# Optimization experiments

Measured on AMD Instinct MI355X. Metric: run time of the kernel, lower is better.

The kernel has to match this reference:

```python
import jax, jax.numpy as jnp
import numpy as np

B, T, F = 16, 2048, 512


def setup_inputs() -> dict:
    key = jax.random.key(0)
    k1, k2, k3 = jax.random.split(key, 3)
    x = jax.random.normal(k1, (B, T, F), dtype=jnp.float32)
    w_aggr = jax.random.normal(k2, (F, 1), dtype=jnp.float32) * 0.02
    b_aggr = jnp.zeros((1,), dtype=jnp.float32)
    # lengths in [T//2, T] to avoid degenerate lengths[0]==0 (torch would div by 0 too)
    seq_len = jax.random.randint(k3, (B,), T // 2, T + 1).astype(jnp.int32)
    return {"x": x, "w_aggr": w_aggr, "b_aggr": b_aggr, "seq_len": seq_len}


def reference(x, w_aggr, b_aggr, seq_len):
    """Valley-detection dynamic segment-mean pooling.

    Faithful to the torch code, but the O(T^2) triangular-mask bmm is
    expressed as the mathematically identical prefix-sum difference:
    bmm(utri[end]-utri[start], v) == cumsum(v)[end] - cumsum(v)[start].
    Output time dim is padded to T (>= dynamic max_counts); padded segment
    rows have start==end==0 -> numerator 0 / clamp -> exactly 0, matching
    the torch zero-padded `valleys` rows.
    """
    Bx, Tx, Fx = x.shape
    wt = jax.nn.sigmoid(x @ w_aggr + b_aggr)[..., 0]          # [B,T] gate weights
    before = jnp.pad(wt[:, :-1], ((0, 0), (1, 0)))            # pad 0 (sigmoid>0 => pos 0 never valley)
    after = jnp.pad(wt[:, 1:], ((0, 0), (0, 1)))              # pad 0 => pos T-1 never valley
    valley = (wt < before) & (wt < after)                     # [B,T] strict local minima
    starts_mask = valley.at[:, 0].set(True)                   # mask[:,0]=True
    ends_mask = valley.at[:, 0].set(False).at[:, -1].set(True)  # mask[:,0]=False; mask[:,-1]=True

    t = jnp.arange(Tx, dtype=jnp.int32)
    bi = jnp.arange(Bx)[:, None]

    def pack(m, vals):
        # left-pack values at True positions into fixed [B,T] (zeros beyond count)
        rank = jnp.cumsum(m, axis=1) - 1
        slot = jnp.where(m, rank, Tx)                         # dump non-selected into slot T
        out = jnp.zeros((Bx, Tx + 1), jnp.int32).at[bi, slot].set(vals)
        return out[:, :Tx], jnp.sum(m, axis=1)

    starts, counts = pack(starts_mask, jnp.broadcast_to(t, (Bx, Tx)))
    end_vals = jnp.broadcast_to(jnp.minimum(t + 2, Tx), (Bx, Tx))  # valley_index_end clipped to length
    ends, _ = pack(ends_mask, end_vals)

    alpha_h = wt[..., None] * x                               # [B,T,F]
    # exclusive->inclusive prefix sums with leading zero row
    cs_ah = jnp.concatenate([jnp.zeros((Bx, 1, Fx), x.dtype), jnp.cumsum(alpha_h, axis=1)], axis=1)
    cs_w = jnp.concatenate([jnp.zeros((Bx, 1), x.dtype), jnp.cumsum(wt, axis=1)], axis=1)

    num = cs_ah[bi, ends] - cs_ah[bi, starts]                 # [B,T,F] segment sums of w*x
    den = jnp.clip(cs_w[bi, ends] - cs_w[bi, starts], 1e-6, None)[..., None]
    pooled = num / den                                        # weighted segment mean

    max_counts = jnp.max(counts)
    lengths = jnp.minimum(seq_len, Tx)
    new_lengths = (lengths.astype(jnp.float32) / lengths[0].astype(jnp.float32)
                   * max_counts.astype(jnp.float32)).astype(jnp.int32)
    new_mask = t[None, :] < new_lengths[:, None]              # [B,T]
    return pooled, new_mask
```

## Files before the change

kernel.cpp:

```cpp
#include <hip/hip_runtime.h>
#include <math.h>

#define BB 16
#define TT 2048
#define FF 512

#define ACTIVE_BLOCKS 4096
#define ZERO_BLOCKS   1024
#define MASK_BLOCKS   32

typedef float v4f __attribute__((ext_vector_type(4)));

__global__ __launch_bounds__(256) void wt_kernel(const float* __restrict__ x,
                                                 const float* __restrict__ w,
                                                 const float* __restrict__ bias,
                                                 float* __restrict__ wt) {
    int gid  = blockIdx.x * 256 + threadIdx.x;
    int row  = gid >> 6;
    int lane = gid & 63;
    const float* xr = x + (size_t)row * FF + lane * 8;
    const float* wr = w + lane * 8;
    float4 a0 = *(const float4*)xr;
    float4 a1 = *(const float4*)(xr + 4);
    float4 w0 = *(const float4*)wr;
    float4 w1 = *(const float4*)(wr + 4);
    float s = a0.x * w0.x + a0.y * w0.y + a0.z * w0.z + a0.w * w0.w
            + a1.x * w1.x + a1.y * w1.y + a1.z * w1.z + a1.w * w1.w;
#pragma unroll
    for (int off = 32; off > 0; off >>= 1) s += __shfl_xor(s, off, 64);
    if (lane == 0) {
        float z = s + bias[0];
        wt[row] = 1.0f / (1.0f + expf(-z));
    }
}

__global__ __launch_bounds__(64) void seg_kernel(const float* __restrict__ wt,
                                                 int* __restrict__ starts,
                                                 int* __restrict__ ends,
                                                 int* __restrict__ counts) {
    int b    = blockIdx.x;
    int lane = threadIdx.x;
    const float* wrow = wt + b * TT;
    float v[32];
    const float4* p = (const float4*)(wrow + lane * 32);
#pragma unroll
    for (int k = 0; k < 8; ++k) {
        float4 f = p[k];
        v[4*k] = f.x; v[4*k+1] = f.y; v[4*k+2] = f.z; v[4*k+3] = f.w;
    }
    float left  = __shfl_up(v[31], 1, 64);
    float right = __shfl_down(v[0], 1, 64);
    unsigned int flags = 0;
#pragma unroll
    for (int k = 0; k < 32; ++k) {
        int t = lane * 32 + k;
        float prev = (k == 0)  ? left  : v[k - 1];
        float next = (k == 31) ? right : v[k + 1];
        bool val = (t > 0) && (t < TT - 1) && (v[k] < prev) && (v[k] < next);
        if (val) flags |= (1u << k);
    }
    int cnt = __popc(flags);
    int inc = cnt;
#pragma unroll
    for (int off = 1; off < 64; off <<= 1) {
        int y = __shfl_up(inc, off, 64);
        if (lane >= off) inc += y;
    }
    int total = __shfl(inc, 63, 64);
    int r = inc - cnt;
    int* sb = starts + b * TT;
    int* eb = ends + b * TT;
    unsigned int f = flags;
    while (f) {
        int k = __ffs(f) - 1;
        f &= f - 1;
        int t = lane * 32 + k;
        sb[r + 1] = t;
        eb[r] = t + 2;
        ++r;
    }
    if (lane == 0) {
        sb[0] = 0;
        eb[total] = TT;
        counts[b] = total + 1;
    }
}

__global__ __launch_bounds__(256) void pool_kernel(const float* __restrict__ x,
                                                   const float* __restrict__ wt,
                                                   const int* __restrict__ starts,
                                                   const int* __restrict__ ends,
                                                   const int* __restrict__ counts,
                                                   const int* __restrict__ seq_len,
                                                   float* __restrict__ out,
                                                   float* __restrict__ mask_out) {
    int blk = blockIdx.x;
    int tid = threadIdx.x;
    v4f zero = (v4f)(0.f);

    if (blk >= ACTIVE_BLOCKS + ZERO_BLOCKS) {
        int idx = (blk - ACTIVE_BLOCKS - ZERO_BLOCKS) * 256 + tid;
        int maxc = 0;
#pragma unroll
        for (int i = 0; i < BB; ++i) maxc = max(maxc, counts[i]);
        float len0 = (float)min(seq_len[0], TT);
#pragma unroll
        for (int r = 0; r < 4; ++r) {
            int i = idx + r * 8192;
            int b = i >> 11, t = i & (TT - 1);
            int nl = (int)((float)min(seq_len[b], TT) / len0 * (float)maxc);
            mask_out[i] = (t < nl) ? 1.0f : 0.0f;
        }
        return;
    }

    if (blk >= ACTIVE_BLOCKS) {
        int zb = blk - ACTIVE_BLOCKS;
        int b  = zb >> 6;
        int j0 = 1024 + (zb & 63) * 16;
        float* base = out + ((size_t)(b * TT + j0) * FF);
        v4f* dst = (v4f*)base + tid * 2;
        __builtin_nontemporal_store(zero, dst);
        __builtin_nontemporal_store(zero, dst + 1);
        return;
    }

    int b    = blk >> 8;
    int wv   = tid >> 6;
    int lane = tid & 63;
    int j    = (blk & 255) * 4 + wv;
    int row  = b * TT + j;
    float* orow = out + (size_t)row * FF + lane * 8;

    v4f acc0 = (v4f)(0.f);
    v4f acc1 = (v4f)(0.f);
    if (j < counts[b]) {
        int s = __builtin_amdgcn_readfirstlane(starts[row]);
        int e = __builtin_amdgcn_readfirstlane(ends[row]);
        const float* xb   = x + (size_t)b * TT * FF + lane * 8;
        const float* wrow = wt + b * TT;
        float den = 0.f;
        for (int t = s; t < e; t += 4) {
            int i1 = (t + 1 < e) ? t + 1 : t;
            int i2 = (t + 2 < e) ? t + 2 : t;
            int i3 = (t + 3 < e) ? t + 3 : t;
            float w0 = wrow[t];
            float w1 = (t + 1 < e) ? wrow[i1] : 0.f;
            float w2 = (t + 2 < e) ? wrow[i2] : 0.f;
            float w3 = (t + 3 < e) ? wrow[i3] : 0.f;
            const v4f* p0 = (const v4f*)(xb + (size_t)t  * FF);
            const v4f* p1 = (const v4f*)(xb + (size_t)i1 * FF);
            const v4f* p2 = (const v4f*)(xb + (size_t)i2 * FF);
            const v4f* p3 = (const v4f*)(xb + (size_t)i3 * FF);
            v4f v00 = p0[0], v01 = p0[1];
            v4f v10 = p1[0], v11 = p1[1];
            v4f v20 = p2[0], v21 = p2[1];
            v4f v30 = p3[0], v31 = p3[1];
            acc0 += w0 * v00; acc1 += w0 * v01;
            acc0 += w1 * v10; acc1 += w1 * v11;
            acc0 += w2 * v20; acc1 += w2 * v21;
            acc0 += w3 * v30; acc1 += w3 * v31;
            den += w0 + w1 + w2 + w3;
        }
        float inv = 1.0f / fmaxf(den, 1e-6f);
        acc0 *= inv; acc1 *= inv;
    }
    __builtin_nontemporal_store(acc0, (v4f*)orow);
    __builtin_nontemporal_store(acc1, (v4f*)(orow + 4));
}

extern "C" void kernel_launch(void* const* d_in, const int* in_sizes, int n_in,
                              void* d_out, int out_size, void* d_ws, size_t ws_size,
                              hipStream_t stream) {
    const float* x       = (const float*)d_in[0];
    const float* w_aggr  = (const float*)d_in[1];
    const float* b_aggr  = (const float*)d_in[2];
    const int*   seq_len = (const int*)d_in[3];

    float* pooled = (float*)d_out;
    float* mask   = (float*)d_out + (size_t)BB * TT * FF;

    float* wt    = (float*)d_ws;
    int* starts  = (int*)((char*)d_ws + (size_t)BB * TT * 4);
    int* ends    = starts + BB * TT;
    int* counts  = ends + BB * TT;

    wt_kernel<<<(BB * TT) / 4, 256, 0, stream>>>(x, w_aggr, b_aggr, wt);
    seg_kernel<<<BB, 64, 0, stream>>>(wt, starts, ends, counts);
    pool_kernel<<<ACTIVE_BLOCKS + ZERO_BLOCKS + MASK_BLOCKS, 256, 0, stream>>>(
        x, wt, starts, ends, counts, seq_len, pooled, mask);
}
```

Baseline: 126.4 us.

## Fuse three kernels into one cooperative persistent kernel with grid syncs

Replaces the separate gate, segmentation and pooling launches with a single cooperative kernel of 1024 blocks that loops over work units and uses grid.sync between phases. The segmentation step now runs with 256 threads per batch and a shared-memory cross-wave scan instead of one 64-lane wave. This removes per-launch overhead and the serialized tiny seg_kernel. In exchange it adds grid-wide barrier cost, caps the grid at 1024 blocks, and leaves most blocks idle during the segmentation phase.

New measurement: 323.9 us. 156% more time.

```diff
diff --git a/kernel.cpp b/kernel.cpp
--- a/kernel.cpp
+++ b/kernel.cpp
@@ -1,172 +1,187 @@
 #include <hip/hip_runtime.h>
+#include <hip/hip_cooperative_groups.h>
 #include <math.h>
+
+namespace cg = cooperative_groups;
 
 #define BB 16
 #define TT 2048
 #define FF 512
 
-#define ACTIVE_BLOCKS 4096
-#define ZERO_BLOCKS   1024
-#define MASK_BLOCKS   32
+#define GRID   1024
+#define NWAVES (GRID * 4)
+
+#define ACTIVE_UNITS 4096
+#define ZERO_UNITS   1024
+#define MASK_UNITS   32
+#define TOTAL_UNITS  (ACTIVE_UNITS + ZERO_UNITS + MASK_UNITS)
 
 typedef float v4f __attribute__((ext_vector_type(4)));
 
-__global__ __launch_bounds__(256) void wt_kernel(const float* __restrict__ x,
-                                                 const float* __restrict__ w,
-                                                 const float* __restrict__ bias,
-                                                 float* __restrict__ wt) {
-    int gid  = blockIdx.x * 256 + threadIdx.x;
-    int row  = gid >> 6;
-    int lane = gid & 63;
-    const float* xr = x + (size_t)row * FF + lane * 8;
-    const float* wr = w + lane * 8;
-    float4 a0 = *(const float4*)xr;
-    float4 a1 = *(const float4*)(xr + 4);
-    float4 w0 = *(const float4*)wr;
-    float4 w1 = *(const float4*)(wr + 4);
-    float s = a0.x * w0.x + a0.y * w0.y + a0.z * w0.z + a0.w * w0.w
-            + a1.x * w1.x + a1.y * w1.y + a1.z * w1.z + a1.w * w1.w;
-#pragma unroll
-    for (int off = 32; off > 0; off >>= 1) s += __shfl_xor(s, off, 64);
-    if (lane == 0) {
-        float z = s + bias[0];
-        wt[row] = 1.0f / (1.0f + expf(-z));
+__global__ __launch_bounds__(256, 4) void fused_kernel(
+    const float* __restrict__ x,
+    const float* __restrict__ w,
+    const float* __restrict__ bias,
+    const int*   __restrict__ seq_len,
+    float* __restrict__ wt,
+    int*   __restrict__ starts,
+    int*   __restrict__ ends,
+    int*   __restrict__ counts,
+    float* __restrict__ out,
+    float* __restrict__ mask_out)
+{
+    cg::grid_group grid = cg::this_grid();
+    __shared__ int wsum[4];
+
+    int tid  = threadIdx.x;
+    int lane = tid & 63;
+    int wv   = tid >> 6;
+
+    {
+        int wgid = blockIdx.x * 4 + wv;
+        const float* wp = w + lane * 8;
+        float4 w0 = *(const float4*)wp;
+        float4 w1 = *(const float4*)(wp + 4);
+        float bz = bias[0];
+#pragma unroll
+        for (int i = 0; i < 8; ++i) {
+            int row = wgid + i * NWAVES;
+            const float* xr = x + (size_t)row * FF + lane * 8;
+            float4 a0 = *(const float4*)xr;
+            float4 a1 = *(const float4*)(xr + 4);
+            float s = a0.x * w0.x + a0.y * w0.y + a0.z * w0.z + a0.w * w0.w
+                    + a1.x * w1.x + a1.y * w1.y + a1.z * w1.z + a1.w * w1.w;
+#pragma unroll
+            for (int off = 32; off > 0; off >>= 1) s += __shfl_xor(s, off, 64);
+            if (lane == 0) {
+                float z = s + bz;
+                wt[row] = 1.0f / (1.0f + expf(-z));
+            }
+        }
     }
-}
-
-__global__ __launch_bounds__(64) void seg_kernel(const float* __restrict__ wt,
-                                                 int* __restrict__ starts,
-                                                 int* __restrict__ ends,
-                                                 int* __restrict__ counts) {
-    int b    = blockIdx.x;
-    int lane = threadIdx.x;
-    const float* wrow = wt + b * TT;
-    float v[32];
-    const float4* p = (const float4*)(wrow + lane * 32);
-#pragma unroll
-    for (int k = 0; k < 8; ++k) {
-        float4 f = p[k];
-        v[4*k] = f.x; v[4*k+1] = f.y; v[4*k+2] = f.z; v[4*k+3] = f.w;
+
+    grid.sync();
+
+    if (blockIdx.x < BB) {
+        int b = blockIdx.x;
+        const float* wrow = wt + b * TT;
+        int t0 = tid * 8;
+        float v[8];
+        float4 f0 = *(const float4*)(wrow + t0);
+        float4 f1 = *(const float4*)(wrow + t0 + 4);
+        v[0] = f0.x; v[1] = f0.y; v[2] = f0.z; v[3] = f0.w;
+        v[4] = f1.x; v[5] = f1.y; v[6] = f1.z; v[7] = f1.w;
+        float left  = (tid > 0)   ? wrow[t0 - 1] : 0.f;
+        float right = (tid < 255) ? wrow[t0 + 8] : 0.f;
+        unsigned int flags = 0;
+#pragma unroll
+        for (int k = 0; k < 8; ++k) {
+            int t = t0 + k;
+            float prev = (k == 0) ? left  : v[k - 1];
+            float next = (k == 7) ? right : v[k + 1];
+            bool val = (t > 0) && (t < TT - 1) && (v[k] < prev) && (v[k] < next);
+            if (val) flags |= (1u << k);
+        }
+        int cnt = __popc(flags);
+        int inc = cnt;
+#pragma unroll
+        for (int off = 1; off < 64; off <<= 1) {
+            int y = __shfl_up(inc, off, 64);
+            if (lane >= off) inc += y;
+        }
+        if (lane == 63) wsum[wv] = inc;
+        __syncthreads();
+        int waveOff = 0;
+#pragma unroll
+        for (int k = 0; k < 4; ++k) if (k < wv) waveOff += wsum[k];
+        int total = wsum[0] + wsum[1] + wsum[2] + wsum[3];
+        int r = waveOff + inc - cnt;
+        int* sb = starts + b * TT;
+        int* eb = ends + b * TT;
+        unsigned int f = flags;
+        while (f) {
+            int k = __ffs(f) - 1;
+            f &= f - 1;
+            int t = t0 + k;
+            sb[r + 1] = t;
+            eb[r] = t + 2;
+            ++r;
+        }
+        if (tid == 0) {
+            sb[0] = 0;
+            eb[total] = TT;
+            counts[b] = total + 1;
+        }
     }
-    float left  = __shfl_up(v[31], 1, 64);
-    float right = __shfl_down(v[0], 1, 64);
-    unsigned int flags = 0;
-#pragma unroll
-    for (int k = 0; k < 32; ++k) {
-        int t = lane * 32 + k;
-        float prev = (k == 0)  ? left  : v[k - 1];
-        float next = (k == 31) ? right : v[k + 1];
-        bool val = (t > 0) && (t < TT - 1) && (v[k] < prev) && (v[k] < next);
-        if (val) flags |= (1u << k);
+
+    grid.sync();
+
+    v4f zero = (v4f)(0.f);
+    for (int u = blockIdx.x; u < TOTAL_UNITS; u += GRID) {
+        if (u < ACTIVE_UNITS) {
+            int b    = u >> 8;
+            int j    = (u & 255) * 4 + wv;
+            int row  = b * TT + j;
+            float* orow = out + (size_t)row * FF + lane * 8;
+
+            v4f acc0 = zero;
+            v4f acc1 = zero;
+            if (j < counts[b]) {
+                int s = __builtin_amdgcn_readfirstlane(starts[row]);
+                int e = __builtin_amdgcn_readfirstlane(ends[row]);
+                const float* xb   = x + (size_t)b * TT * FF + lane * 8;
+                const float* wrow = wt + b * TT;
+                float den = 0.f;
+                for (int t = s; t < e; t += 4) {
+                    int i1 = (t + 1 < e) ? t + 1 : t;
+                    int i2 = (t + 2 < e) ? t + 2 : t;
+                    int i3 = (t + 3 < e) ? t + 3 : t;
+                    float w0 = wrow[t];
+                    float w1 = (t + 1 < e) ? wrow[i1] : 0.f;
+                    float w2 = (t + 2 < e) ? wrow[i2] : 0.f;
+                    float w3 = (t + 3 < e) ? wrow[i3] : 0.f;
+                    const v4f* p0 = (const v4f*)(xb + (size_t)t  * FF);
+                    const v4f* p1 = (const v4f*)(xb + (size_t)i1 * FF);
+                    const v4f* p2 = (const v4f*)(xb + (size_t)i2 * FF);
+                    const v4f* p3 = (const v4f*)(xb + (size_t)i3 * FF);
+                    v4f v00 = p0[0], v01 = p0[1];
+                    v4f v10 = p1[0], v11 = p1[1];
+                    v4f v20 = p2[0], v21 = p2[1];
+                    v4f v30 = p3[0], v31 = p3[1];
+                    acc0 += w0 * v00; acc1 += w0 * v01;
+                    acc0 += w1 * v10; acc1 += w1 * v11;
+                    acc0 += w2 * v20; acc1 += w2 * v21;
+                    acc0 += w3 * v30; acc1 += w3 * v31;
+                    den += w0 + w1 + w2 + w3;
+                }
+                float inv = 1.0f / fmaxf(den, 1e-6f);
+                acc0 *= inv; acc1 *= inv;
+            }
+            __builtin_nontemporal_store(acc0, (v4f*)orow);
+            __builtin_nontemporal_store(acc1, (v4f*)(orow + 4));
+        } else if (u < ACTIVE_UNITS + ZERO_UNITS) {
+            int zb = u - ACTIVE_UNITS;
+            int b  = zb >> 6;
+            int j0 = 1024 + (zb & 63) * 16;
+            float* base = out + ((size_t)(b * TT + j0) * FF);
+            v4f* dst = (v4f*)base + tid * 2;
+            __builtin_nontemporal_store(zero, dst);
+            __builtin_nontemporal_store(zero, dst + 1);
+        } else {
+            int idx = (u - ACTIVE_UNITS - ZERO_UNITS) * 256 + tid;
+            int maxc = 0;
+#pragma unroll
+            for (int i = 0; i < BB; ++i) maxc = max(maxc, counts[i]);
+            float len0 = (float)min(seq_len[0], TT);
+#pragma unroll
+            for (int r = 0; r < 4; ++r) {
+                int i = idx + r * 8192;
+                int b = i >> 11, t = i & (TT - 1);
+                int nl = (int)((float)min(seq_len[b], TT) / len0 * (float)maxc);
+                mask_out[i] = (t < nl) ? 1.0f : 0.0f;
+            }
+        }
     }
-    int cnt = __popc(flags);
-    int inc = cnt;
-#pragma unroll
-    for (int off = 1; off < 64; off <<= 1) {
-        int y = __shfl_up(inc, off, 64);
-        if (lane >= off) inc += y;
-    }
-    int total = __shfl(inc, 63, 64);
-    int r = inc - cnt;
-    int* sb = starts + b * TT;
-    int* eb = ends + b * TT;
-    unsigned int f = flags;
-    while (f) {
-        int k = __ffs(f) - 1;
-        f &= f - 1;
-        int t = lane * 32 + k;
-        sb[r + 1] = t;
-        eb[r] = t + 2;
-        ++r;
-    }
-    if (lane == 0) {
-        sb[0] = 0;
-        eb[total] = TT;
-        counts[b] = total + 1;
-    }
-}
-
-__global__ __launch_bounds__(256) void pool_kernel(const float* __restrict__ x,
-                                                   const float* __restrict__ wt,
-                                                   const int* __restrict__ starts,
-                                                   const int* __restrict__ ends,
-                                                   const int* __restrict__ counts,
-                                                   const int* __restrict__ seq_len,
-                                                   float* __restrict__ out,
-                                                   float* __restrict__ mask_out) {
-    int blk = blockIdx.x;
-    int tid = threadIdx.x;
-    v4f zero = (v4f)(0.f);
-
-    if (blk >= ACTIVE_BLOCKS + ZERO_BLOCKS) {
-        int idx = (blk - ACTIVE_BLOCKS - ZERO_BLOCKS) * 256 + tid;
-        int maxc = 0;
-#pragma unroll
-        for (int i = 0; i < BB; ++i) maxc = max(maxc, counts[i]);
-        float len0 = (float)min(seq_len[0], TT);
-#pragma unroll
-        for (int r = 0; r < 4; ++r) {
-            int i = idx + r * 8192;
-            int b = i >> 11, t = i & (TT - 1);
-            int nl = (int)((float)min(seq_len[b], TT) / len0 * (float)maxc);
-            mask_out[i] = (t < nl) ? 1.0f : 0.0f;
-        }
-        return;
-    }
-
-    if (blk >= ACTIVE_BLOCKS) {
-        int zb = blk - ACTIVE_BLOCKS;
-        int b  = zb >> 6;
-        int j0 = 1024 + (zb & 63) * 16;
-        float* base = out + ((size_t)(b * TT + j0) * FF);
-        v4f* dst = (v4f*)base + tid * 2;
-        __builtin_nontemporal_store(zero, dst);
-        __builtin_nontemporal_store(zero, dst + 1);
-        return;
-    }
-
-    int b    = blk >> 8;
-    int wv   = tid >> 6;
-    int lane = tid & 63;
-    int j    = (blk & 255) * 4 + wv;
-    int row  = b * TT + j;
-    float* orow = out + (size_t)row * FF + lane * 8;
-
-    v4f acc0 = (v4f)(0.f);
-    v4f acc1 = (v4f)(0.f);
-    if (j < counts[b]) {
-        int s = __builtin_amdgcn_readfirstlane(starts[row]);
-        int e = __builtin_amdgcn_readfirstlane(ends[row]);
-        const float* xb   = x + (size_t)b * TT * FF + lane * 8;
-        const float* wrow = wt + b * TT;
-        float den = 0.f;
-        for (int t = s; t < e; t += 4) {
-            int i1 = (t + 1 < e) ? t + 1 : t;
-            int i2 = (t + 2 < e) ? t + 2 : t;
-            int i3 = (t + 3 < e) ? t + 3 : t;
-            float w0 = wrow[t];
-            float w1 = (t + 1 < e) ? wrow[i1] : 0.f;
-            float w2 = (t + 2 < e) ? wrow[i2] : 0.f;
-            float w3 = (t + 3 < e) ? wrow[i3] : 0.f;
-            const v4f* p0 = (const v4f*)(xb + (size_t)t  * FF);
-            const v4f* p1 = (const v4f*)(xb + (size_t)i1 * FF);
-            const v4f* p2 = (const v4f*)(xb + (size_t)i2 * FF);
-            const v4f* p3 = (const v4f*)(xb + (size_t)i3 * FF);
-            v4f v00 = p0[0], v01 = p0[1];
-            v4f v10 = p1[0], v11 = p1[1];
-            v4f v20 = p2[0], v21 = p2[1];
-            v4f v30 = p3[0], v31 = p3[1];
-            acc0 += w0 * v00; acc1 += w0 * v01;
-            acc0 += w1 * v10; acc1 += w1 * v11;
-            acc0 += w2 * v20; acc1 += w2 * v21;
-            acc0 += w3 * v30; acc1 += w3 * v31;
-            den += w0 + w1 + w2 + w3;
-        }
-        float inv = 1.0f / fmaxf(den, 1e-6f);
-        acc0 *= inv; acc1 *= inv;
-    }
-    __builtin_nontemporal_store(acc0, (v4f*)orow);
-    __builtin_nontemporal_store(acc1, (v4f*)(orow + 4));
 }
 
 extern "C" void kernel_launch(void* const* d_in, const int* in_sizes, int n_in,
@@ -185,8 +200,9 @@
     int* ends    = starts + BB * TT;
     int* counts  = ends + BB * TT;
 
-    wt_kernel<<<(BB * TT) / 4, 256, 0, stream>>>(x, w_aggr, b_aggr, wt);
-    seg_kernel<<<BB, 64, 0, stream>>>(wt, starts, ends, counts);
-    pool_kernel<<<ACTIVE_BLOCKS + ZERO_BLOCKS + MASK_BLOCKS, 256, 0, stream>>>(
-        x, wt, starts, ends, counts, seq_len, pooled, mask);
+    void* args[] = {(void*)&x, (void*)&w_aggr, (void*)&b_aggr, (void*)&seq_len,
+                    (void*)&wt, (void*)&starts, (void*)&ends, (void*)&counts,
+                    (void*)&pooled, (void*)&mask};
+    hipLaunchCooperativeKernel(reinterpret_cast<void*>(fused_kernel),
+                               dim3(GRID), dim3(256), args, 0, stream);
 }
```

## Fuse gate and valley-flag computation, derive segment bounds in pool kernel

Applied to the files above, without the earlier changes.

Merges the sigmoid gate kernel and the serial single-wave segmentation kernel into one kernel. Each block computes gates for a 32-step chunk, including halo rows, and writes a per-chunk valley bitmask. The pool kernel rebuilds counts and segment start/end from these bitmasks using a wave prefix sum and ballot search. This removes one launch and the low-parallelism 16-block segment pass. In exchange, every pool block and the mask blocks repeat the popcount/scan work, and halo rows are recomputed per chunk.

Result: no change. 126.3 us (-0.1%).

```diff
diff --git a/kernel.cpp b/kernel.cpp
--- a/kernel.cpp
+++ b/kernel.cpp
@@ -5,92 +5,101 @@
 #define TT 2048
 #define FF 512
 
-#define ACTIVE_BLOCKS 4096
-#define ZERO_BLOCKS   1024
-#define MASK_BLOCKS   32
+#define CHUNK  32
+#define NCHUNK (TT / CHUNK)
+
+#define ACTIVE_UNITS 4096
+#define ZERO_UNITS   1024
+#define MASK_UNITS   32
 
 typedef float v4f __attribute__((ext_vector_type(4)));
 
-__global__ __launch_bounds__(256) void wt_kernel(const float* __restrict__ x,
-                                                 const float* __restrict__ w,
-                                                 const float* __restrict__ bias,
-                                                 float* __restrict__ wt) {
-    int gid  = blockIdx.x * 256 + threadIdx.x;
-    int row  = gid >> 6;
-    int lane = gid & 63;
-    const float* xr = x + (size_t)row * FF + lane * 8;
-    const float* wr = w + lane * 8;
-    float4 a0 = *(const float4*)xr;
-    float4 a1 = *(const float4*)(xr + 4);
-    float4 w0 = *(const float4*)wr;
-    float4 w1 = *(const float4*)(wr + 4);
-    float s = a0.x * w0.x + a0.y * w0.y + a0.z * w0.z + a0.w * w0.w
-            + a1.x * w1.x + a1.y * w1.y + a1.z * w1.z + a1.w * w1.w;
-#pragma unroll
-    for (int off = 32; off > 0; off >>= 1) s += __shfl_xor(s, off, 64);
-    if (lane == 0) {
-        float z = s + bias[0];
-        wt[row] = 1.0f / (1.0f + expf(-z));
-    }
-}
-
-__global__ __launch_bounds__(64) void seg_kernel(const float* __restrict__ wt,
-                                                 int* __restrict__ starts,
-                                                 int* __restrict__ ends,
-                                                 int* __restrict__ counts) {
-    int b    = blockIdx.x;
-    int lane = threadIdx.x;
-    const float* wrow = wt + b * TT;
-    float v[32];
-    const float4* p = (const float4*)(wrow + lane * 32);
-#pragma unroll
-    for (int k = 0; k < 8; ++k) {
-        float4 f = p[k];
-        v[4*k] = f.x; v[4*k+1] = f.y; v[4*k+2] = f.z; v[4*k+3] = f.w;
-    }
-    float left  = __shfl_up(v[31], 1, 64);
-    float right = __shfl_down(v[0], 1, 64);
-    unsigned int flags = 0;
-#pragma unroll
-    for (int k = 0; k < 32; ++k) {
-        int t = lane * 32 + k;
-        float prev = (k == 0)  ? left  : v[k - 1];
-        float next = (k == 31) ? right : v[k + 1];
-        bool val = (t > 0) && (t < TT - 1) && (v[k] < prev) && (v[k] < next);
-        if (val) flags |= (1u << k);
-    }
-    int cnt = __popc(flags);
-    int inc = cnt;
-#pragma unroll
-    for (int off = 1; off < 64; off <<= 1) {
-        int y = __shfl_up(inc, off, 64);
-        if (lane >= off) inc += y;
-    }
-    int total = __shfl(inc, 63, 64);
-    int r = inc - cnt;
-    int* sb = starts + b * TT;
-    int* eb = ends + b * TT;
-    unsigned int f = flags;
-    while (f) {
-        int k = __ffs(f) - 1;
-        f &= f - 1;
-        int t = lane * 32 + k;
-        sb[r + 1] = t;
-        eb[r] = t + 2;
-        ++r;
-    }
-    if (lane == 0) {
-        sb[0] = 0;
-        eb[total] = TT;
-        counts[b] = total + 1;
+__global__ __launch_bounds__(256) void wtflag_kernel(const float* __restrict__ x,
+                                                     const float* __restrict__ w,
+                                                     const float* __restrict__ bias,
+                                                     float* __restrict__ wt,
+                                                     unsigned int* __restrict__ flags) {
+    __shared__ float arr[CHUNK + 2];
+    int blk  = blockIdx.x;
+    int b    = blk >> 6;
+    int c    = blk & 63;
+    int t0   = c * CHUNK;
+    int tid  = threadIdx.x;
+    int wv   = tid >> 6;
+    int lane = tid & 63;
+
+    const float* wp = w + lane * 8;
+    float4 w0 = *(const float4*)wp;
+    float4 w1 = *(const float4*)(wp + 4);
+    float bz = bias[0];
+
+    int rbase = b * TT + t0 + wv * 8;
+    const float* xr0 = x + (size_t)rbase * FF + lane * 8;
+    float sv[8];
+#pragma unroll
+    for (int i = 0; i < 8; ++i) {
+        const float* xr = xr0 + (size_t)i * FF;
+        float4 a0 = *(const float4*)xr;
+        float4 a1 = *(const float4*)(xr + 4);
+        sv[i] = a0.x * w0.x + a0.y * w0.y + a0.z * w0.z + a0.w * w0.w
+              + a1.x * w1.x + a1.y * w1.y + a1.z * w1.z + a1.w * w1.w;
+    }
+#pragma unroll
+    for (int i = 0; i < 8; ++i) {
+        float s = sv[i];
+#pragma unroll
+        for (int off = 32; off > 0; off >>= 1) s += __shfl_xor(s, off, 64);
+        float val = 1.0f / (1.0f + expf(-(s + bz)));
+        if (lane == 0) {
+            arr[1 + wv * 8 + i] = val;
+            wt[rbase + i] = val;
+        }
+    }
+
+    if (wv == 0) {
+        if (t0 > 0) {
+            const float* xr = x + (size_t)(b * TT + t0 - 1) * FF + lane * 8;
+            float4 a0 = *(const float4*)xr;
+            float4 a1 = *(const float4*)(xr + 4);
+            float s = a0.x * w0.x + a0.y * w0.y + a0.z * w0.z + a0.w * w0.w
+                    + a1.x * w1.x + a1.y * w1.y + a1.z * w1.z + a1.w * w1.w;
+#pragma unroll
+            for (int off = 32; off > 0; off >>= 1) s += __shfl_xor(s, off, 64);
+            if (lane == 0) arr[0] = 1.0f / (1.0f + expf(-(s + bz)));
+        } else if (lane == 0) arr[0] = 0.f;
+    }
+    if (wv == 3) {
+        if (t0 + CHUNK < TT) {
+            const float* xr = x + (size_t)(b * TT + t0 + CHUNK) * FF + lane * 8;
+            float4 a0 = *(const float4*)xr;
+            float4 a1 = *(const float4*)(xr + 4);
+            float s = a0.x * w0.x + a0.y * w0.y + a0.z * w0.z + a0.w * w0.w
+                    + a1.x * w1.x + a1.y * w1.y + a1.z * w1.z + a1.w * w1.w;
+#pragma unroll
+            for (int off = 32; off > 0; off >>= 1) s += __shfl_xor(s, off, 64);
+            if (lane == 0) arr[CHUNK + 1] = 1.0f / (1.0f + expf(-(s + bz)));
+        } else if (lane == 0) arr[CHUNK + 1] = 0.f;
+    }
+
+    __syncthreads();
+
+    if (tid < 64) {
+        bool val = false;
+        if (tid < CHUNK) {
+            int t = t0 + tid;
+            float cv = arr[1 + tid];
+            float pv = arr[tid];
+            float nv = arr[2 + tid];
+            val = (t > 0) && (t < TT - 1) && (cv < pv) && (cv < nv);
+        }
+        unsigned long long bm = __ballot(val);
+        if (tid == 0) flags[b * NCHUNK + c] = (unsigned int)bm;
     }
 }
 
 __global__ __launch_bounds__(256) void pool_kernel(const float* __restrict__ x,
                                                    const float* __restrict__ wt,
-                                                   const int* __restrict__ starts,
-                                                   const int* __restrict__ ends,
-                                                   const int* __restrict__ counts,
+                                                   const unsigned int* __restrict__ flags,
                                                    const int* __restrict__ seq_len,
                                                    float* __restrict__ out,
                                                    float* __restrict__ mask_out) {
@@ -98,12 +107,20 @@
     int tid = threadIdx.x;
     v4f zero = (v4f)(0.f);
 
-    if (blk >= ACTIVE_BLOCKS + ZERO_BLOCKS) {
-        int idx = (blk - ACTIVE_BLOCKS - ZERO_BLOCKS) * 256 + tid;
+    if (blk >= ACTIVE_UNITS + ZERO_UNITS) {
+        __shared__ int cnts_lds[BB];
+        int s4 = 0;
+#pragma unroll
+        for (int q = 0; q < 4; ++q) s4 += __popc(flags[tid * 4 + q]);
+#pragma unroll
+        for (int off = 1; off < 16; off <<= 1) s4 += __shfl_xor(s4, off, 64);
+        if ((tid & 15) == 0) cnts_lds[tid >> 4] = s4 + 1;
+        __syncthreads();
         int maxc = 0;
 #pragma unroll
-        for (int i = 0; i < BB; ++i) maxc = max(maxc, counts[i]);
+        for (int i = 0; i < BB; ++i) maxc = max(maxc, cnts_lds[i]);
         float len0 = (float)min(seq_len[0], TT);
+        int idx = (blk - ACTIVE_UNITS - ZERO_UNITS) * 256 + tid;
 #pragma unroll
         for (int r = 0; r < 4; ++r) {
             int i = idx + r * 8192;
@@ -114,8 +131,8 @@
         return;
     }
 
-    if (blk >= ACTIVE_BLOCKS) {
-        int zb = blk - ACTIVE_BLOCKS;
+    if (blk >= ACTIVE_UNITS) {
+        int zb = blk - ACTIVE_UNITS;
         int b  = zb >> 6;
         int j0 = 1024 + (zb & 63) * 16;
         float* base = out + ((size_t)(b * TT + j0) * FF);
@@ -132,11 +149,37 @@
     int row  = b * TT + j;
     float* orow = out + (size_t)row * FF + lane * 8;
 
-    v4f acc0 = (v4f)(0.f);
-    v4f acc1 = (v4f)(0.f);
-    if (j < counts[b]) {
-        int s = __builtin_amdgcn_readfirstlane(starts[row]);
-        int e = __builtin_amdgcn_readfirstlane(ends[row]);
+    const unsigned int* fb = flags + b * NCHUNK;
+    unsigned int wd = fb[lane];
+    int pc  = __popc(wd);
+    int inc = pc;
+#pragma unroll
+    for (int off = 1; off < 64; off <<= 1) {
+        int y = __shfl_up(inc, off, 64);
+        if (lane >= off) inc += y;
+    }
+    int exc = inc - pc;
+    int k   = __shfl(inc, 63, 64);
+    int cnt = k + 1;
+
+    v4f acc0 = zero;
+    v4f acc1 = zero;
+    if (j < cnt) {
+        auto findv = [&](int jj) -> int {
+            bool has = (exc < jj) && (jj <= exc + pc);
+            unsigned long long m = __ballot(has);
+            int ls = (int)(__ffsll(m) - 1);
+            unsigned int wsel = __shfl(wd, ls, 64);
+            int base = __shfl(exc, ls, 64);
+            int need = jj - base;
+            for (int q = 1; q < need; ++q) wsel &= wsel - 1;
+            return ls * 32 + (__ffs(wsel) - 1);
+        };
+        int s = (j == 0) ? 0  : findv(j);
+        int e = (j == k) ? TT : findv(j + 1) + 2;
+        s = __builtin_amdgcn_readfirstlane(s);
+        e = __builtin_amdgcn_readfirstlane(e);
+
         const float* xb   = x + (size_t)b * TT * FF + lane * 8;
         const float* wrow = wt + b * TT;
         float den = 0.f;
@@ -180,13 +223,10 @@
     float* pooled = (float*)d_out;
     float* mask   = (float*)d_out + (size_t)BB * TT * FF;
 
-    float* wt    = (float*)d_ws;
-    int* starts  = (int*)((char*)d_ws + (size_t)BB * TT * 4);
-    int* ends    = starts + BB * TT;
-    int* counts  = ends + BB * TT;
-
-    wt_kernel<<<(BB * TT) / 4, 256, 0, stream>>>(x, w_aggr, b_aggr, wt);
-    seg_kernel<<<BB, 64, 0, stream>>>(wt, starts, ends, counts);
-    pool_kernel<<<ACTIVE_BLOCKS + ZERO_BLOCKS + MASK_BLOCKS, 256, 0, stream>>>(
-        x, wt, starts, ends, counts, seq_len, pooled, mask);
+    float*        wt    = (float*)d_ws;
+    unsigned int* flags = (unsigned int*)((char*)d_ws + (size_t)BB * TT * 4);
+
+    wtflag_kernel<<<BB * NCHUNK, 256, 0, stream>>>(x, w_aggr, b_aggr, wt, flags);
+    pool_kernel<<<ACTIVE_UNITS + ZERO_UNITS + MASK_UNITS, 256, 0, stream>>>(
+        x, wt, flags, seq_len, pooled, mask);
 }
```
